# Kernel optimization log

Measured on AMD Instinct MI355X. Metric: run time of the kernel, lower is better.

The kernel has to match this reference:

```python
import jax, jax.numpy as jnp
import numpy as np

B, I, H, AH, AI = 4096, 1024, 1024, 128, 16
EPS = 1e-5  # nn.LayerNorm default


def _ln(x, w, b):
    mu = jnp.mean(x, -1, keepdims=True)
    var = jnp.mean((x - mu) ** 2, -1, keepdims=True)
    return (x - mu) * jax.lax.rsqrt(var + EPS) * w + b


def setup_inputs() -> dict:
    key = jax.random.key(0)
    ks = jax.random.split(key, 12)
    d = {}
    d['x'] = jax.random.normal(ks[0], (B, I), jnp.float32)
    d['total_h'] = jax.random.normal(ks[1], (B, H + AH), jnp.float32)
    d['total_c'] = jax.random.normal(ks[2], (B, H + AH), jnp.float32)
    # main cell params
    d['w_ih'] = jax.random.normal(ks[3], (4 * H, I), jnp.float32) * 0.02
    d['w_hh'] = jax.random.normal(ks[4], (4 * H, H), jnp.float32) * 0.02
    d['b_ih'] = jnp.zeros((4 * H,), jnp.float32)
    d['b_hh'] = jnp.zeros((4 * H,), jnp.float32)
    d['ln_i_w'] = jnp.ones((4 * H,), jnp.float32); d['ln_i_b'] = jnp.zeros((4 * H,), jnp.float32)
    d['ln_h_w'] = jnp.ones((4 * H,), jnp.float32); d['ln_h_b'] = jnp.zeros((4 * H,), jnp.float32)
    d['ln_c_w'] = jnp.ones((H,), jnp.float32); d['ln_c_b'] = jnp.zeros((H,), jnp.float32)
    # 8 AdaptiveNorm modules, stacked on leading axis (order ix,jx,fx,ox,ih,jh,fh,oh)
    d['norm_zw_w'] = jax.random.normal(ks[5], (8, AI, AH), jnp.float32) * 0.05
    d['norm_zw_b'] = jnp.ones((8, AI), jnp.float32)
    d['norm_alpha_w'] = jax.random.normal(ks[6], (8, H, AI), jnp.float32) * (0.1 / AI)
    # 8 AdaptiveBias modules, stacked (order ixb,jxb,fxb,oxb,ihb,jhb,fhb,ohb)
    d['bias_zb_w'] = jax.random.normal(ks[7], (8, AI, AH), jnp.float32) * 0.01
    d['bias_beta_w'] = jax.random.normal(ks[8], (8, H, AI), jnp.float32) * 0.01
    # adaptive LayerNormLSTMCell (input = I+H, hidden = AH)
    d['a_w_ih'] = jax.random.normal(ks[9], (4 * AH, I + H), jnp.float32) * 0.02
    d['a_w_hh'] = jax.random.normal(ks[10], (4 * AH, AH), jnp.float32) * 0.02
    d['a_ln_i_w'] = jnp.ones((4 * AH,), jnp.float32); d['a_ln_i_b'] = jnp.zeros((4 * AH,), jnp.float32)
    d['a_ln_h_w'] = jnp.ones((4 * AH,), jnp.float32); d['a_ln_h_b'] = jnp.zeros((4 * AH,), jnp.float32)
    d['a_ln_c_w'] = jnp.ones((AH,), jnp.float32); d['a_ln_c_b'] = jnp.zeros((AH,), jnp.float32)
    return d


def _forward(x, total_h, total_c, w_ih, w_hh, b_ih, b_hh, ln_i_w, ln_i_b,
             ln_h_w, ln_h_b, ln_c_w, ln_c_b, norm_zw_w, norm_zw_b,
             norm_alpha_w, bias_zb_w, bias_beta_w, a_w_ih, a_w_hh,
             a_ln_i_w, a_ln_i_b, a_ln_h_w, a_ln_h_b, a_ln_c_w, a_ln_c_b):
    hx, ah = total_h[:, :H], total_h[:, H:]
    cx, ac = total_c[:, :H], total_c[:, H:]
    # ---- adaptive LayerNormLSTMCell (hypernetwork) ----
    ai = jnp.concatenate([x, hx], axis=1)                     # [B, I+H]
    ig = _ln(ai @ a_w_ih.T, a_ln_i_w, a_ln_i_b)               # [B, 4*AH]
    hg = _ln(ah @ a_w_hh.T, a_ln_h_w, a_ln_h_b)
    g = ig + hg
    gi, gf, gj, go = jnp.split(g, 4, axis=1)                  # ingate, forget, cell, out
    acy = _ln(jax.nn.sigmoid(gf) * ac + jax.nn.sigmoid(gi) * jnp.tanh(gj), a_ln_c_w, a_ln_c_b)
    ada = jax.nn.sigmoid(go) * jnp.tanh(acy)                  # adaptive_output [B, AH]
    # ---- 8 AdaptiveNorm scales + 8 AdaptiveBias offsets, batched ----
    zw = jnp.einsum('ba,sia->bsi', ada, norm_zw_w) + norm_zw_b  # [B,8,AI]
    alpha = jnp.einsum('bsi,shi->bsh', zw, norm_alpha_w)        # [B,8,H]
    zb = jnp.einsum('ba,sia->bsi', ada, bias_zb_w)              # [B,8,AI]
    beta = jnp.einsum('bsi,shi->bsh', zb, bias_beta_w)          # [B,8,H]
    xh = (x @ w_ih.T).reshape(-1, 4, H)                         # chunks ix,jx,fx,ox
    hh = (hx @ w_hh.T).reshape(-1, 4, H)                        # chunks ih,jh,fh,oh
    in_g = (xh * alpha[:, :4] + b_ih.reshape(4, H) + beta[:, :4]).reshape(-1, 4 * H)
    hid_g = (hh * alpha[:, 4:] + b_hh.reshape(4, H) + beta[:, 4:]).reshape(-1, 4 * H)
    # ---- cell_operate ----
    gates = _ln(in_g, ln_i_w, ln_i_b) + _ln(hid_g, ln_h_w, ln_h_b)
    i, j, f, o = jnp.split(gates, 4, axis=1)                  # in, cell, forget, out
    cy = _ln(jax.nn.sigmoid(f) * cx + jax.nn.sigmoid(i) * jnp.tanh(j), ln_c_w, ln_c_b)
    hy = jax.nn.sigmoid(o) * jnp.tanh(cy)
    new_total_h = jnp.concatenate([hy, ada], axis=1)
    new_total_c = jnp.concatenate([cy, acy], axis=1)
    return hy, new_total_h, new_total_c


def reference(x, total_h, total_c, w_ih, w_hh, b_ih, b_hh, ln_i_w, ln_i_b,
              ln_h_w, ln_h_b, ln_c_w, ln_c_b, norm_zw_w, norm_zw_b,
              norm_alpha_w, bias_zb_w, bias_beta_w, a_w_ih, a_w_hh,
              a_ln_i_w, a_ln_i_b, a_ln_h_w, a_ln_h_b, a_ln_c_w, a_ln_c_b):
    return _forward(x, total_h, total_c, w_ih, w_hh, b_ih, b_hh, ln_i_w, ln_i_b,
                    ln_h_w, ln_h_b, ln_c_w, ln_c_b, norm_zw_w, norm_zw_b,
                    norm_alpha_w, bias_zb_w, bias_beta_w, a_w_ih, a_w_hh,
                    a_ln_i_w, a_ln_i_b, a_ln_h_w, a_ln_h_b, a_ln_c_w, a_ln_c_b)
```

## Files before the change

kernel.cpp:

```cpp
#include <hip/hip_runtime.h>
#include <cstdint>
#include <cstddef>


#define B_   4096
#define I_   1024
#define H_   1024
#define AH_  128
#define AI_  16
#define G4_  4096
#define EPS_ 1e-5f

#define OUT_TH ((size_t)B_ * H_)
#define OUT_TC (OUT_TH + (size_t)B_ * (H_ + AH_))

typedef short s16x8 __attribute__((ext_vector_type(8)));
typedef float f32x4 __attribute__((ext_vector_type(4)));

__device__ __forceinline__ unsigned short f2bf_rn(float f) {
    unsigned int u = __builtin_bit_cast(unsigned int, f);
    unsigned int r = u + 0x7FFFu + ((u >> 16) & 1u);
    return (unsigned short)(r >> 16);
}
__device__ __forceinline__ float bf2f(unsigned short h) {
    unsigned int u = ((unsigned int)h) << 16;
    return __builtin_bit_cast(float, u);
}
__device__ __forceinline__ float sigf(float x) { return 1.0f / (1.0f + expf(-x)); }

__device__ __forceinline__ void gld16(const void* g, void* l) {
    __builtin_amdgcn_global_load_lds(
        (const __attribute__((address_space(1))) unsigned int*)g,
        (__attribute__((address_space(3))) unsigned int*)l,
        16, 0, 0);
}

__global__ void split3_kernel(const float* __restrict__ src, int srcStride, int srcOff,
                              long total, int K,
                              unsigned short* __restrict__ dst, int dstStride,
                              int offHiA, int offHiB, int offLo) {
    long idx = (long)blockIdx.x * blockDim.x + threadIdx.x;
    if (idx >= total) return;
    int r = (int)(idx / K);
    int k = (int)(idx - (long)r * K);
    float v = src[(size_t)r * srcStride + srcOff + k];
    unsigned short hu = f2bf_rn(v);
    unsigned short lu = f2bf_rn(v - bf2f(hu));
    size_t base = (size_t)r * dstStride;
    dst[base + offHiA + k] = hu;
    dst[base + offHiB + k] = hu;
    dst[base + offLo  + k] = lu;
}

__launch_bounds__(256, 2)
__global__ void gemm_bt_bf16(const unsigned short* __restrict__ A0,
                             const unsigned short* __restrict__ A1,
                             int kSplit, int lda,
                             const unsigned short* __restrict__ W, int ldw,
                             float* __restrict__ C, int ldc, int K) {
    __shared__ __align__(16) unsigned short As[128 * 32];
    __shared__ __align__(16) unsigned short Bs[128 * 32];
    const int tid  = threadIdx.x;
    const int lane = tid & 63;
    const int w    = tid >> 6;
    const int wr   = w >> 1, wc = w & 1;
    const int bx   = blockIdx.x, by = blockIdx.y;
    const int l15  = lane & 15;
    const int lk   = (lane >> 4) * 8;

    f32x4 acc[4][4] = {};

    for (int kt = 0; kt < K; kt += 32) {
        const unsigned short* Ab = (kt < kSplit) ? (A0 + kt) : (A1 + (kt - kSplit));
        const unsigned short* Wb = W + kt;
#pragma unroll
        for (int it = 0; it < 2; ++it) {
            int q = it * 256 + tid;
            int row = q >> 2, c8 = (q & 3) * 8;
            gld16(Ab + (size_t)(by * 128 + row) * lda + c8,
                  (char*)As + (size_t)(it * 256 + w * 64) * 16);
        }
#pragma unroll
        for (int it = 0; it < 2; ++it) {
            int q = it * 256 + tid;
            int row = q >> 2, c8 = (q & 3) * 8;
            gld16(Wb + (size_t)(bx * 128 + row) * ldw + c8,
                  (char*)Bs + (size_t)(it * 256 + w * 64) * 16);
        }
        __syncthreads();

        s16x8 afr[4], bfr[4];
#pragma unroll
        for (int m = 0; m < 4; ++m)
            afr[m] = *(const s16x8*)&As[(wr * 64 + m * 16 + l15) * 32 + lk];
#pragma unroll
        for (int n = 0; n < 4; ++n)
            bfr[n] = *(const s16x8*)&Bs[(wc * 64 + n * 16 + l15) * 32 + lk];
#pragma unroll
        for (int m = 0; m < 4; ++m)
#pragma unroll
            for (int n = 0; n < 4; ++n)
                acc[m][n] = __builtin_amdgcn_mfma_f32_16x16x32_bf16(
                    afr[m], bfr[n], acc[m][n], 0, 0, 0);
        __syncthreads();
    }

    const int r0 = by * 128 + wr * 64;
    const int c0 = bx * 128 + wc * 64;
    const int rl = (lane >> 4) * 4;
#pragma unroll
    for (int m = 0; m < 4; ++m)
#pragma unroll
        for (int n = 0; n < 4; ++n)
#pragma unroll
            for (int j = 0; j < 4; ++j)
                C[(size_t)(r0 + m * 16 + rl + j) * ldc + c0 + n * 16 + l15] = acc[m][n][j];
}

__launch_bounds__(64)
__global__ void adaptive_gates_kernel(const float* __restrict__ IG, const float* __restrict__ HG,
                                      const float* __restrict__ total_c,
                                      const float* __restrict__ alniw, const float* __restrict__ alnib,
                                      const float* __restrict__ alnhw, const float* __restrict__ alnhb,
                                      const float* __restrict__ alncw, const float* __restrict__ alncb,
                                      const float* __restrict__ zw_w, const float* __restrict__ zw_b,
                                      const float* __restrict__ zb_w,
                                      float* __restrict__ ZW, float* __restrict__ ZB,
                                      float* __restrict__ out) {
    const int b    = blockIdx.x;
    const int lane = threadIdx.x;
    __shared__ float ada_lds[AH_];

    float ig[8], hg[8];
    const float* igp = IG + (size_t)b * 512 + lane * 8;
    const float* hgp = HG + (size_t)b * 512 + lane * 8;
    float sI = 0, qI = 0, sH = 0, qH = 0;
#pragma unroll
    for (int j = 0; j < 8; ++j) {
        ig[j] = igp[j]; sI += ig[j]; qI += ig[j] * ig[j];
        hg[j] = hgp[j]; sH += hg[j]; qH += hg[j] * hg[j];
    }
#pragma unroll
    for (int m = 1; m < 64; m <<= 1) {
        sI += __shfl_xor(sI, m); qI += __shfl_xor(qI, m);
        sH += __shfl_xor(sH, m); qH += __shfl_xor(qH, m);
    }
    const float muI = sI * (1.0f / 512.0f);
    const float rI  = rsqrtf(qI * (1.0f / 512.0f) - muI * muI + EPS_);
    const float muH = sH * (1.0f / 512.0f);
    const float rH  = rsqrtf(qH * (1.0f / 512.0f) - muH * muH + EPS_);

    float g[8];
#pragma unroll
    for (int j = 0; j < 8; ++j) {
        int c = lane * 8 + j;
        g[j] = (ig[j] - muI) * rI * alniw[c] + alnib[c]
             + (hg[j] - muH) * rH * alnhw[c] + alnhb[c];
    }

    const int l15 = lane & 15;
    float cp[8], gov[8];
    float s = 0, q = 0;
#pragma unroll
    for (int j = 0; j < 8; ++j) {
        float giv = __shfl(g[j], l15);
        float gfv = __shfl(g[j], 16 + l15);
        float gjv = __shfl(g[j], 32 + l15);
        gov[j]    = __shfl(g[j], 48 + l15);
        int a = l15 * 8 + j;
        float ac = total_c[(size_t)b * (H_ + AH_) + H_ + a];
        cp[j] = sigf(gfv) * ac + sigf(giv) * tanhf(gjv);
        s += cp[j]; q += cp[j] * cp[j];
    }
#pragma unroll
    for (int m = 1; m < 16; m <<= 1) { s += __shfl_xor(s, m); q += __shfl_xor(q, m); }
    const float mu = s * (1.0f / 128.0f);
    const float rs = rsqrtf(q * (1.0f / 128.0f) - mu * mu + EPS_);

    float adav[8], acyv[8];
#pragma unroll
    for (int j = 0; j < 8; ++j) {
        int a = l15 * 8 + j;
        acyv[j] = (cp[j] - mu) * rs * alncw[a] + alncb[a];
        adav[j] = sigf(gov[j]) * tanhf(acyv[j]);
    }
    if (lane < 16) {
#pragma unroll
        for (int j = 0; j < 8; ++j) {
            int a = lane * 8 + j;
            ada_lds[a] = adav[j];
            out[OUT_TH + (size_t)b * (H_ + AH_) + H_ + a] = adav[j];
            out[OUT_TC + (size_t)b * (H_ + AH_) + H_ + a] = acyv[j];
        }
    }
    __syncthreads();

#pragma unroll
    for (int t = 0; t < 2; ++t) {
        int idx = lane * 2 + t;
        const float* wz = zw_w + (size_t)idx * AH_;
        const float* wb = zb_w + (size_t)idx * AH_;
        float az = 0, ab = 0;
        for (int a = 0; a < AH_; ++a) {
            float ad = ada_lds[a];
            az += ad * wz[a];
            ab += ad * wb[a];
        }
        ZW[(size_t)b * 128 + idx] = az + zw_b[idx];
        ZB[(size_t)b * 128 + idx] = ab;
    }
}

__launch_bounds__(512)
__global__ void scale_stats_kernel(float* __restrict__ XH, float* __restrict__ HH,
                                   const float* __restrict__ ZW, const float* __restrict__ ZB,
                                   const float* __restrict__ aw, const float* __restrict__ bw,
                                   const float* __restrict__ b_ih, const float* __restrict__ b_hh,
                                   float* __restrict__ STATS) {
    const int tid  = threadIdx.x;
    const int lane = tid & 63;
    const int w    = tid >> 6;
    const int b0   = blockIdx.x * 8;

    __shared__ float zwl[8 * 128], zbl[8 * 128];
    __shared__ float part[8][8][4];
    __shared__ float tot[8][4];

    for (int t = tid; t < 1024; t += 512) {
        int r = t >> 7, si = t & 127;
        zwl[t] = ZW[(size_t)(b0 + r) * 128 + si];
        zbl[t] = ZB[(size_t)(b0 + r) * 128 + si];
    }
    __syncthreads();

    float sI[8] = {}, qI[8] = {}, sH[8] = {}, qH[8] = {};

    for (int strip = w; strip < 128; strip += 8) {
        const bool isIn = strip < 64;
        const int  c    = (isIn ? strip : strip - 64) * 64 + lane;
        const int  se   = (c >> 10) + (isIn ? 0 : 4);
        float*       X    = isIn ? XH : HH;
        const float* bias = isIn ? b_ih : b_hh;
        const int    h    = c & 1023;

        const f32x4* awp = (const f32x4*)(aw + ((size_t)se * 1024 + h) * 16);
        const f32x4* bwp = (const f32x4*)(bw + ((size_t)se * 1024 + h) * 16);
        f32x4 a0 = awp[0], a1 = awp[1], a2 = awp[2], a3 = awp[3];
        f32x4 w0 = bwp[0], w1 = bwp[1], w2 = bwp[2], w3 = bwp[3];
        const float bc = bias[c];

#pragma unroll
        for (int r = 0; r < 8; ++r) {
            const float* z  = &zwl[r * 128 + se * 16];
            const float* zb = &zbl[r * 128 + se * 16];
            float alpha = a0[0]*z[0]  + a0[1]*z[1]  + a0[2]*z[2]  + a0[3]*z[3]
                        + a1[0]*z[4]  + a1[1]*z[5]  + a1[2]*z[6]  + a1[3]*z[7]
                        + a2[0]*z[8]  + a2[1]*z[9]  + a2[2]*z[10] + a2[3]*z[11]
                        + a3[0]*z[12] + a3[1]*z[13] + a3[2]*z[14] + a3[3]*z[15];
            float beta  = w0[0]*zb[0]  + w0[1]*zb[1]  + w0[2]*zb[2]  + w0[3]*zb[3]
                        + w1[0]*zb[4]  + w1[1]*zb[5]  + w1[2]*zb[6]  + w1[3]*zb[7]
                        + w2[0]*zb[8]  + w2[1]*zb[9]  + w2[2]*zb[10] + w2[3]*zb[11]
                        + w3[0]*zb[12] + w3[1]*zb[13] + w3[2]*zb[14] + w3[3]*zb[15];
            size_t off = (size_t)(b0 + r) * G4_ + c;
            float v = X[off] * alpha + bc + beta;
            X[off] = v;
            if (isIn) { sI[r] += v; qI[r] += v * v; }
            else      { sH[r] += v; qH[r] += v * v; }
        }
    }

#pragma unroll
    for (int r = 0; r < 8; ++r) {
#pragma unroll
        for (int m = 1; m < 64; m <<= 1) {
            sI[r] += __shfl_xor(sI[r], m); qI[r] += __shfl_xor(qI[r], m);
            sH[r] += __shfl_xor(sH[r], m); qH[r] += __shfl_xor(qH[r], m);
        }
        if (lane == 0) {
            part[w][r][0] = sI[r]; part[w][r][1] = qI[r];
            part[w][r][2] = sH[r]; part[w][r][3] = qH[r];
        }
    }
    __syncthreads();
    if (tid < 32) {
        int r = tid >> 2, cmp = tid & 3;
        float t = 0;
        for (int ww = 0; ww < 8; ++ww) t += part[ww][r][cmp];
        tot[r][cmp] = t;
    }
    __syncthreads();
    if (tid < 8) {
        int r = tid;
        float muI = tot[r][0] * (1.0f / 4096.0f);
        float vI  = tot[r][1] * (1.0f / 4096.0f) - muI * muI;
        float muH = tot[r][2] * (1.0f / 4096.0f);
        float vH  = tot[r][3] * (1.0f / 4096.0f) - muH * muH;
        f32x4 st = { muI, rsqrtf(vI + EPS_), muH, rsqrtf(vH + EPS_) };
        *(f32x4*)(STATS + (size_t)(b0 + r) * 4) = st;
    }
}

__launch_bounds__(256)
__global__ void final_gates_kernel(const float* __restrict__ XH, const float* __restrict__ HH,
                                   const float* __restrict__ STATS,
                                   const float* __restrict__ lniw, const float* __restrict__ lnib,
                                   const float* __restrict__ lnhw, const float* __restrict__ lnhb,
                                   const float* __restrict__ lncw, const float* __restrict__ lncb,
                                   const float* __restrict__ total_c,
                                   float* __restrict__ out) {
    const int b = blockIdx.x, tid = threadIdx.x;
    const int lane = tid & 63, w = tid >> 6;
    __shared__ float red[4][2];

    const f32x4 st = *(const f32x4*)(STATS + (size_t)b * 4);
    const int h0 = tid * 4;

    float gg[4][4];
#pragma unroll
    for (int s = 0; s < 4; ++s) {
        int c = s * 1024 + h0;
        f32x4 xi = *(const f32x4*)(XH + (size_t)b * G4_ + c);
        f32x4 hi = *(const f32x4*)(HH + (size_t)b * G4_ + c);
        f32x4 wi = *(const f32x4*)(lniw + c);
        f32x4 bi = *(const f32x4*)(lnib + c);
        f32x4 wh = *(const f32x4*)(lnhw + c);
        f32x4 bh = *(const f32x4*)(lnhb + c);
#pragma unroll
        for (int e = 0; e < 4; ++e)
            gg[s][e] = (xi[e] - st[0]) * st[1] * wi[e] + bi[e]
                     + (hi[e] - st[2]) * st[3] * wh[e] + bh[e];
    }

    float cp[4], ov[4];
    float s_ = 0, q_ = 0;
#pragma unroll
    for (int e = 0; e < 4; ++e) {
        float iv = gg[0][e], jv = gg[1][e], fv = gg[2][e];
        ov[e] = gg[3][e];
        float cx = total_c[(size_t)b * (H_ + AH_) + h0 + e];
        cp[e] = sigf(fv) * cx + sigf(iv) * tanhf(jv);
        s_ += cp[e]; q_ += cp[e] * cp[e];
    }
#pragma unroll
    for (int m = 1; m < 64; m <<= 1) { s_ += __shfl_xor(s_, m); q_ += __shfl_xor(q_, m); }
    if (lane == 0) { red[w][0] = s_; red[w][1] = q_; }
    __syncthreads();
    float S = red[0][0] + red[1][0] + red[2][0] + red[3][0];
    float Q = red[0][1] + red[1][1] + red[2][1] + red[3][1];
    float mu = S * (1.0f / 1024.0f);
    float rs = rsqrtf(Q * (1.0f / 1024.0f) - mu * mu + EPS_);

    f32x4 hyv, cyv;
#pragma unroll
    for (int e = 0; e < 4; ++e) {
        int h = h0 + e;
        float cy = (cp[e] - mu) * rs * lncw[h] + lncb[h];
        float hy = sigf(ov[e]) * tanhf(cy);
        cyv[e] = cy; hyv[e] = hy;
    }
    *(f32x4*)(out + (size_t)b * H_ + h0)                        = hyv;
    *(f32x4*)(out + OUT_TH + (size_t)b * (H_ + AH_) + h0)       = hyv;
    *(f32x4*)(out + OUT_TC + (size_t)b * (H_ + AH_) + h0)       = cyv;
}

extern "C" void kernel_launch(void* const* d_in, const int* in_sizes, int n_in,
                              void* d_out, int out_size, void* d_ws, size_t ws_size,
                              hipStream_t stream) {
    const float* x          = (const float*)d_in[0];
    const float* total_h    = (const float*)d_in[1];
    const float* total_c    = (const float*)d_in[2];
    const float* w_ih       = (const float*)d_in[3];
    const float* w_hh       = (const float*)d_in[4];
    const float* b_ih       = (const float*)d_in[5];
    const float* b_hh       = (const float*)d_in[6];
    const float* ln_i_w     = (const float*)d_in[7];
    const float* ln_i_b     = (const float*)d_in[8];
    const float* ln_h_w     = (const float*)d_in[9];
    const float* ln_h_b     = (const float*)d_in[10];
    const float* ln_c_w     = (const float*)d_in[11];
    const float* ln_c_b     = (const float*)d_in[12];
    const float* norm_zw_w  = (const float*)d_in[13];
    const float* norm_zw_b  = (const float*)d_in[14];
    const float* norm_alpha_w = (const float*)d_in[15];
    const float* bias_zb_w  = (const float*)d_in[16];
    const float* bias_beta_w = (const float*)d_in[17];
    const float* a_w_ih     = (const float*)d_in[18];
    const float* a_w_hh     = (const float*)d_in[19];
    const float* a_ln_i_w   = (const float*)d_in[20];
    const float* a_ln_i_b   = (const float*)d_in[21];
    const float* a_ln_h_w   = (const float*)d_in[22];
    const float* a_ln_h_b   = (const float*)d_in[23];
    const float* a_ln_c_w   = (const float*)d_in[24];
    const float* a_ln_c_b   = (const float*)d_in[25];
    float* out = (float*)d_out;

    char* ws = (char*)d_ws;
    unsigned short* XA  = (unsigned short*)(ws + 0);
    unsigned short* HXA = (unsigned short*)(ws + 25165824);
    unsigned short* WIH = (unsigned short*)(ws + 50331648);
    unsigned short* WHH = (unsigned short*)(ws + 75497472);
    unsigned short* WAI = (unsigned short*)(ws + 100663296);
    unsigned short* AHS = (unsigned short*)(ws + 106954752);
    unsigned short* WAH = (unsigned short*)(ws + 110100480);
    float* IG    = (float*)(ws + 110493696);
    float* HG    = (float*)(ws + 118882304);
    float* XHp   = (float*)(ws + 127270912);
    float* HHp   = (float*)(ws + 194379776);
    float* ZW    = (float*)(ws + 261488640);
    float* ZB    = (float*)(ws + 263585792);
    float* STATS = (float*)(ws + 265682944);

    auto grid1 = [](long n) { return dim3((unsigned)((n + 255) / 256)); };

    split3_kernel<<<grid1(4096L*1024), 256, 0, stream>>>(x,       1024, 0,    4096L*1024, 1024, XA,  3072, 0, 1024, 2048);
    split3_kernel<<<grid1(4096L*1024), 256, 0, stream>>>(total_h, 1152, 0,    4096L*1024, 1024, HXA, 3072, 0, 1024, 2048);
    split3_kernel<<<grid1(4096L*128),  256, 0, stream>>>(total_h, 1152, 1024, 4096L*128,  128,  AHS, 384,  0, 128,  256);
    split3_kernel<<<grid1(4096L*1024), 256, 0, stream>>>(w_ih,    1024, 0,    4096L*1024, 1024, WIH, 3072, 0, 2048, 1024);
    split3_kernel<<<grid1(4096L*1024), 256, 0, stream>>>(w_hh,    1024, 0,    4096L*1024, 1024, WHH, 3072, 0, 2048, 1024);
    split3_kernel<<<grid1(512L*1024),  256, 0, stream>>>(a_w_ih,  2048, 0,    512L*1024,  1024, WAI,        6144, 0, 2048, 1024);
    split3_kernel<<<grid1(512L*1024),  256, 0, stream>>>(a_w_ih,  2048, 1024, 512L*1024,  1024, WAI + 3072, 6144, 0, 2048, 1024);
    split3_kernel<<<grid1(512L*128),   256, 0, stream>>>(a_w_hh,  128,  0,    512L*128,   128,  WAH, 384,  0, 256,  128);

    const int BIG = 1 << 30;
    gemm_bt_bf16<<<dim3(512/128, 4096/128), 256, 0, stream>>>(XA, HXA, 3072, 3072, WAI, 6144, IG, 512, 6144);
    gemm_bt_bf16<<<dim3(512/128, 4096/128), 256, 0, stream>>>(AHS, AHS, BIG, 384, WAH, 384, HG, 512, 384);
    gemm_bt_bf16<<<dim3(4096/128, 4096/128), 256, 0, stream>>>(XA,  XA,  BIG, 3072, WIH, 3072, XHp, 4096, 3072);
    gemm_bt_bf16<<<dim3(4096/128, 4096/128), 256, 0, stream>>>(HXA, HXA, BIG, 3072, WHH, 3072, HHp, 4096, 3072);

    adaptive_gates_kernel<<<4096, 64, 0, stream>>>(IG, HG, total_c,
        a_ln_i_w, a_ln_i_b, a_ln_h_w, a_ln_h_b, a_ln_c_w, a_ln_c_b,
        norm_zw_w, norm_zw_b, bias_zb_w, ZW, ZB, out);

    scale_stats_kernel<<<512, 512, 0, stream>>>(XHp, HHp, ZW, ZB,
        norm_alpha_w, bias_beta_w, b_ih, b_hh, STATS);

    final_gates_kernel<<<4096, 256, 0, stream>>>(XHp, HHp, STATS,
        ln_i_w, ln_i_b, ln_h_w, ln_h_b, ln_c_w, ln_c_b, total_c, out);
}
```

Measured before the change: 823.6 us.

## Vectorize bf16 split, drop duplicated hi copy, swizzle GEMM blocks, split adaptive GEMM

Result: faster. 668.6 us (-18.8%).

```diff
diff --git a/kernel.cpp b/kernel.cpp
--- a/kernel.cpp
+++ b/kernel.cpp
@@ -7,7 +7,6 @@
 #define I_   1024
 #define H_   1024
 #define AH_  128
-#define AI_  16
 #define G4_  4096
 #define EPS_ 1e-5f
 
@@ -35,44 +34,69 @@
         16, 0, 0);
 }
 
-__global__ void split3_kernel(const float* __restrict__ src, int srcStride, int srcOff,
-                              long total, int K,
+__global__ void split8_kernel(const float* __restrict__ src, int srcStride, int srcOff,
+                              long nThreads, int kshift,
                               unsigned short* __restrict__ dst, int dstStride,
-                              int offHiA, int offHiB, int offLo) {
-    long idx = (long)blockIdx.x * blockDim.x + threadIdx.x;
-    if (idx >= total) return;
-    int r = (int)(idx / K);
-    int k = (int)(idx - (long)r * K);
-    float v = src[(size_t)r * srcStride + srcOff + k];
-    unsigned short hu = f2bf_rn(v);
-    unsigned short lu = f2bf_rn(v - bf2f(hu));
-    size_t base = (size_t)r * dstStride;
-    dst[base + offHiA + k] = hu;
-    dst[base + offHiB + k] = hu;
-    dst[base + offLo  + k] = lu;
+                              int offHi, int offLo) {
+    long t = (long)blockIdx.x * blockDim.x + threadIdx.x;
+    if (t >= nThreads) return;
+    int r  = (int)(t >> kshift);
+    int kk = ((int)t & ((1 << kshift) - 1)) * 8;
+    const float* sp = src + (size_t)r * srcStride + srcOff + kk;
+    f32x4 v0 = *(const f32x4*)sp;
+    f32x4 v1 = *(const f32x4*)(sp + 4);
+    float v[8] = {v0[0], v0[1], v0[2], v0[3], v1[0], v1[1], v1[2], v1[3]};
+    s16x8 hi, lo;
+#pragma unroll
+    for (int j = 0; j < 8; ++j) {
+        unsigned short hu = f2bf_rn(v[j]);
+        unsigned short lu = f2bf_rn(v[j] - bf2f(hu));
+        hi[j] = (short)hu; lo[j] = (short)lu;
+    }
+    size_t base = (size_t)r * dstStride + kk;
+    *(s16x8*)(dst + base + offHi) = hi;
+    *(s16x8*)(dst + base + offLo) = lo;
+}
+
+__global__ void transpose128_kernel(const float* __restrict__ zw_w, const float* __restrict__ zb_w,
+                                    float* __restrict__ ZWT, float* __restrict__ ZBT) {
+    int t = blockIdx.x * 256 + threadIdx.x;
+    int idx = t >> 7, a = t & 127;
+    ZWT[a * 128 + idx] = zw_w[idx * 128 + a];
+    ZBT[a * 128 + idx] = zb_w[idx * 128 + a];
 }
 
 __launch_bounds__(256, 2)
 __global__ void gemm_bt_bf16(const unsigned short* __restrict__ A0,
                              const unsigned short* __restrict__ A1,
-                             int kSplit, int lda,
-                             const unsigned short* __restrict__ W, int ldw,
-                             float* __restrict__ C, int ldc, int K) {
+                             int lda,
+                             const unsigned short* __restrict__ W, int ldw, int wzOff,
+                             float* __restrict__ C, int ldc, long czOff,
+                             int K, int kA1, int kW1) {
     __shared__ __align__(16) unsigned short As[128 * 32];
     __shared__ __align__(16) unsigned short Bs[128 * 32];
+    const unsigned short* A  = blockIdx.z ? A1 : A0;
+    const unsigned short* Wp = W + (size_t)blockIdx.z * wzOff;
+    float* Cp = C + (size_t)blockIdx.z * czOff;
+
+    const int gx = gridDim.x;
+    int lin = blockIdx.y * gx + blockIdx.x;
+    const int cpx = (gx * gridDim.y) >> 3;
+    lin = (lin & 7) * cpx + (lin >> 3);
+    const int bx = lin % gx, by = lin / gx;
+
     const int tid  = threadIdx.x;
     const int lane = tid & 63;
     const int w    = tid >> 6;
     const int wr   = w >> 1, wc = w & 1;
-    const int bx   = blockIdx.x, by = blockIdx.y;
     const int l15  = lane & 15;
     const int lk   = (lane >> 4) * 8;
 
     f32x4 acc[4][4] = {};
 
     for (int kt = 0; kt < K; kt += 32) {
-        const unsigned short* Ab = (kt < kSplit) ? (A0 + kt) : (A1 + (kt - kSplit));
-        const unsigned short* Wb = W + kt;
+        const unsigned short* Ab = A  + (kt < kA1 ? kt : kt - kA1);
+        const unsigned short* Wb = Wp + (kt < kW1 ? kt : kt - kW1);
 #pragma unroll
         for (int it = 0; it < 2; ++it) {
             int q = it * 256 + tid;
@@ -114,17 +138,18 @@
         for (int n = 0; n < 4; ++n)
 #pragma unroll
             for (int j = 0; j < 4; ++j)
-                C[(size_t)(r0 + m * 16 + rl + j) * ldc + c0 + n * 16 + l15] = acc[m][n][j];
+                Cp[(size_t)(r0 + m * 16 + rl + j) * ldc + c0 + n * 16 + l15] = acc[m][n][j];
 }
 
 __launch_bounds__(64)
-__global__ void adaptive_gates_kernel(const float* __restrict__ IG, const float* __restrict__ HG,
+__global__ void adaptive_gates_kernel(const float* __restrict__ IGa, const float* __restrict__ IGb,
+                                      const float* __restrict__ HG,
                                       const float* __restrict__ total_c,
                                       const float* __restrict__ alniw, const float* __restrict__ alnib,
                                       const float* __restrict__ alnhw, const float* __restrict__ alnhb,
                                       const float* __restrict__ alncw, const float* __restrict__ alncb,
-                                      const float* __restrict__ zw_w, const float* __restrict__ zw_b,
-                                      const float* __restrict__ zb_w,
+                                      const float* __restrict__ ZWT, const float* __restrict__ zw_b,
+                                      const float* __restrict__ ZBT,
                                       float* __restrict__ ZW, float* __restrict__ ZB,
                                       float* __restrict__ out) {
     const int b    = blockIdx.x;
@@ -132,13 +157,14 @@
     __shared__ float ada_lds[AH_];
 
     float ig[8], hg[8];
-    const float* igp = IG + (size_t)b * 512 + lane * 8;
-    const float* hgp = HG + (size_t)b * 512 + lane * 8;
+    const float* ipa = IGa + (size_t)b * 512 + lane * 8;
+    const float* ipb = IGb + (size_t)b * 512 + lane * 8;
+    const float* hgp = HG  + (size_t)b * 512 + lane * 8;
     float sI = 0, qI = 0, sH = 0, qH = 0;
 #pragma unroll
     for (int j = 0; j < 8; ++j) {
-        ig[j] = igp[j]; sI += ig[j]; qI += ig[j] * ig[j];
-        hg[j] = hgp[j]; sH += hg[j]; qH += hg[j] * hg[j];
+        ig[j] = ipa[j] + ipb[j]; sI += ig[j]; qI += ig[j] * ig[j];
+        hg[j] = hgp[j];          sH += hg[j]; qH += hg[j] * hg[j];
     }
 #pragma unroll
     for (int m = 1; m < 64; m <<= 1) {
@@ -195,20 +221,20 @@
     }
     __syncthreads();
 
-#pragma unroll
-    for (int t = 0; t < 2; ++t) {
-        int idx = lane * 2 + t;
-        const float* wz = zw_w + (size_t)idx * AH_;
-        const float* wb = zb_w + (size_t)idx * AH_;
-        float az = 0, ab = 0;
-        for (int a = 0; a < AH_; ++a) {
-            float ad = ada_lds[a];
-            az += ad * wz[a];
-            ab += ad * wb[a];
-        }
-        ZW[(size_t)b * 128 + idx] = az + zw_b[idx];
-        ZB[(size_t)b * 128 + idx] = ab;
-    }
+    float az0 = 0, az1 = 0, ab0 = 0, ab1 = 0;
+#pragma unroll 4
+    for (int a = 0; a < 128; ++a) {
+        float ad = ada_lds[a];
+        float2 wz = *(const float2*)&ZWT[a * 128 + lane * 2];
+        float2 wb = *(const float2*)&ZBT[a * 128 + lane * 2];
+        az0 += ad * wz.x; az1 += ad * wz.y;
+        ab0 += ad * wb.x; ab1 += ad * wb.y;
+    }
+    const int i0 = lane * 2, i1 = lane * 2 + 1;
+    ZW[(size_t)b * 128 + i0] = az0 + zw_b[i0];
+    ZW[(size_t)b * 128 + i1] = az1 + zw_b[i1];
+    ZB[(size_t)b * 128 + i0] = ab0;
+    ZB[(size_t)b * 128 + i1] = ab1;
 }
 
 __launch_bounds__(512)
@@ -222,7 +248,7 @@
     const int w    = tid >> 6;
     const int b0   = blockIdx.x * 8;
 
-    __shared__ float zwl[8 * 128], zbl[8 * 128];
+    __shared__ __align__(16) float zwl[8 * 128], zbl[8 * 128];
     __shared__ float part[8][8][4];
     __shared__ float tot[8][4];
 
@@ -251,16 +277,18 @@
 
 #pragma unroll
         for (int r = 0; r < 8; ++r) {
-            const float* z  = &zwl[r * 128 + se * 16];
-            const float* zb = &zbl[r * 128 + se * 16];
-            float alpha = a0[0]*z[0]  + a0[1]*z[1]  + a0[2]*z[2]  + a0[3]*z[3]
-                        + a1[0]*z[4]  + a1[1]*z[5]  + a1[2]*z[6]  + a1[3]*z[7]
-                        + a2[0]*z[8]  + a2[1]*z[9]  + a2[2]*z[10] + a2[3]*z[11]
-                        + a3[0]*z[12] + a3[1]*z[13] + a3[2]*z[14] + a3[3]*z[15];
-            float beta  = w0[0]*zb[0]  + w0[1]*zb[1]  + w0[2]*zb[2]  + w0[3]*zb[3]
-                        + w1[0]*zb[4]  + w1[1]*zb[5]  + w1[2]*zb[6]  + w1[3]*zb[7]
-                        + w2[0]*zb[8]  + w2[1]*zb[9]  + w2[2]*zb[10] + w2[3]*zb[11]
-                        + w3[0]*zb[12] + w3[1]*zb[13] + w3[2]*zb[14] + w3[3]*zb[15];
+            const f32x4* zp = (const f32x4*)&zwl[r * 128 + se * 16];
+            const f32x4* yp = (const f32x4*)&zbl[r * 128 + se * 16];
+            f32x4 z0 = zp[0], z1 = zp[1], z2 = zp[2], z3 = zp[3];
+            f32x4 y0 = yp[0], y1 = yp[1], y2 = yp[2], y3 = yp[3];
+            float alpha = a0[0]*z0[0] + a0[1]*z0[1] + a0[2]*z0[2] + a0[3]*z0[3]
+                        + a1[0]*z1[0] + a1[1]*z1[1] + a1[2]*z1[2] + a1[3]*z1[3]
+                        + a2[0]*z2[0] + a2[1]*z2[1] + a2[2]*z2[2] + a2[3]*z2[3]
+                        + a3[0]*z3[0] + a3[1]*z3[1] + a3[2]*z3[2] + a3[3]*z3[3];
+            float beta  = w0[0]*y0[0] + w0[1]*y0[1] + w0[2]*y0[2] + w0[3]*y0[3]
+                        + w1[0]*y1[0] + w1[1]*y1[1] + w1[2]*y1[2] + w1[3]*y1[3]
+                        + w2[0]*y2[0] + w2[1]*y2[1] + w2[2]*y2[2] + w2[3]*y2[3]
+                        + w3[0]*y3[0] + w3[1]*y3[1] + w3[2]*y3[2] + w3[3]*y3[3];
             size_t off = (size_t)(b0 + r) * G4_ + c;
             float v = X[off] * alpha + bc + beta;
             X[off] = v;
@@ -358,9 +386,9 @@
         float hy = sigf(ov[e]) * tanhf(cy);
         cyv[e] = cy; hyv[e] = hy;
     }
-    *(f32x4*)(out + (size_t)b * H_ + h0)                        = hyv;
-    *(f32x4*)(out + OUT_TH + (size_t)b * (H_ + AH_) + h0)       = hyv;
-    *(f32x4*)(out + OUT_TC + (size_t)b * (H_ + AH_) + h0)       = cyv;
+    *(f32x4*)(out + (size_t)b * H_ + h0)                  = hyv;
+    *(f32x4*)(out + OUT_TH + (size_t)b * (H_ + AH_) + h0) = hyv;
+    *(f32x4*)(out + OUT_TC + (size_t)b * (H_ + AH_) + h0) = cyv;
 }
 
 extern "C" void kernel_launch(void* const* d_in, const int* in_sizes, int n_in,
@@ -396,40 +424,42 @@
 
     char* ws = (char*)d_ws;
     unsigned short* XA  = (unsigned short*)(ws + 0);
-    unsigned short* HXA = (unsigned short*)(ws + 25165824);
-    unsigned short* WIH = (unsigned short*)(ws + 50331648);
-    unsigned short* WHH = (unsigned short*)(ws + 75497472);
-    unsigned short* WAI = (unsigned short*)(ws + 100663296);
-    unsigned short* AHS = (unsigned short*)(ws + 106954752);
-    unsigned short* WAH = (unsigned short*)(ws + 110100480);
-    float* IG    = (float*)(ws + 110493696);
-    float* HG    = (float*)(ws + 118882304);
-    float* XHp   = (float*)(ws + 127270912);
-    float* HHp   = (float*)(ws + 194379776);
-    float* ZW    = (float*)(ws + 261488640);
-    float* ZB    = (float*)(ws + 263585792);
-    float* STATS = (float*)(ws + 265682944);
-
-    auto grid1 = [](long n) { return dim3((unsigned)((n + 255) / 256)); };
-
-    split3_kernel<<<grid1(4096L*1024), 256, 0, stream>>>(x,       1024, 0,    4096L*1024, 1024, XA,  3072, 0, 1024, 2048);
-    split3_kernel<<<grid1(4096L*1024), 256, 0, stream>>>(total_h, 1152, 0,    4096L*1024, 1024, HXA, 3072, 0, 1024, 2048);
-    split3_kernel<<<grid1(4096L*128),  256, 0, stream>>>(total_h, 1152, 1024, 4096L*128,  128,  AHS, 384,  0, 128,  256);
-    split3_kernel<<<grid1(4096L*1024), 256, 0, stream>>>(w_ih,    1024, 0,    4096L*1024, 1024, WIH, 3072, 0, 2048, 1024);
-    split3_kernel<<<grid1(4096L*1024), 256, 0, stream>>>(w_hh,    1024, 0,    4096L*1024, 1024, WHH, 3072, 0, 2048, 1024);
-    split3_kernel<<<grid1(512L*1024),  256, 0, stream>>>(a_w_ih,  2048, 0,    512L*1024,  1024, WAI,        6144, 0, 2048, 1024);
-    split3_kernel<<<grid1(512L*1024),  256, 0, stream>>>(a_w_ih,  2048, 1024, 512L*1024,  1024, WAI + 3072, 6144, 0, 2048, 1024);
-    split3_kernel<<<grid1(512L*128),   256, 0, stream>>>(a_w_hh,  128,  0,    512L*128,   128,  WAH, 384,  0, 256,  128);
-
-    const int BIG = 1 << 30;
-    gemm_bt_bf16<<<dim3(512/128, 4096/128), 256, 0, stream>>>(XA, HXA, 3072, 3072, WAI, 6144, IG, 512, 6144);
-    gemm_bt_bf16<<<dim3(512/128, 4096/128), 256, 0, stream>>>(AHS, AHS, BIG, 384, WAH, 384, HG, 512, 384);
-    gemm_bt_bf16<<<dim3(4096/128, 4096/128), 256, 0, stream>>>(XA,  XA,  BIG, 3072, WIH, 3072, XHp, 4096, 3072);
-    gemm_bt_bf16<<<dim3(4096/128, 4096/128), 256, 0, stream>>>(HXA, HXA, BIG, 3072, WHH, 3072, HHp, 4096, 3072);
-
-    adaptive_gates_kernel<<<4096, 64, 0, stream>>>(IG, HG, total_c,
+    unsigned short* HXA = (unsigned short*)(ws + 16777216);
+    unsigned short* WIH = (unsigned short*)(ws + 33554432);
+    unsigned short* WHH = (unsigned short*)(ws + 50331648);
+    unsigned short* WAI = (unsigned short*)(ws + 67108864);
+    unsigned short* AHS = (unsigned short*)(ws + 71303168);
+    unsigned short* WAH = (unsigned short*)(ws + 73400320);
+    float* IG    = (float*)(ws + 73662464);
+    float* HG    = (float*)(ws + 90439680);
+    float* XHp   = (float*)(ws + 98828288);
+    float* HHp   = (float*)(ws + 165937152);
+    float* ZW    = (float*)(ws + 233046016);
+    float* ZB    = (float*)(ws + 235143168);
+    float* STATS = (float*)(ws + 237240320);
+    float* ZWT   = (float*)(ws + 237305856);
+    float* ZBT   = (float*)(ws + 237371392);
+
+    auto grid8 = [](long n) { return dim3((unsigned)((n / 8 + 255) / 256)); };
+
+    split8_kernel<<<grid8(4096L*1024), 256, 0, stream>>>(x,       1024, 0,    4096L*128, 7, XA,  2048, 0, 1024);
+    split8_kernel<<<grid8(4096L*1024), 256, 0, stream>>>(total_h, 1152, 0,    4096L*128, 7, HXA, 2048, 0, 1024);
+    split8_kernel<<<grid8(4096L*128),  256, 0, stream>>>(total_h, 1152, 1024, 4096L*16,  4, AHS, 256,  0, 128);
+    split8_kernel<<<grid8(4096L*1024), 256, 0, stream>>>(w_ih,    1024, 0,    4096L*128, 7, WIH, 2048, 0, 1024);
+    split8_kernel<<<grid8(4096L*1024), 256, 0, stream>>>(w_hh,    1024, 0,    4096L*128, 7, WHH, 2048, 0, 1024);
+    split8_kernel<<<grid8(512L*1024),  256, 0, stream>>>(a_w_ih,  2048, 0,    512L*128,  7, WAI, 4096, 0,    1024);
+    split8_kernel<<<grid8(512L*1024),  256, 0, stream>>>(a_w_ih,  2048, 1024, 512L*128,  7, WAI, 4096, 2048, 3072);
+    split8_kernel<<<grid8(512L*128),   256, 0, stream>>>(a_w_hh,  128,  0,    512L*16,   4, WAH, 256,  0, 128);
+    transpose128_kernel<<<64, 256, 0, stream>>>(norm_zw_w, bias_zb_w, ZWT, ZBT);
+
+    gemm_bt_bf16<<<dim3(4, 32, 2), 256, 0, stream>>>(XA, HXA, 2048, WAI, 4096, 2048, IG, 512, 4096L*512, 3072, 1024, 2048);
+    gemm_bt_bf16<<<dim3(4, 32, 1), 256, 0, stream>>>(AHS, AHS, 256, WAH, 256, 0, HG, 512, 0, 384, 128, 256);
+    gemm_bt_bf16<<<dim3(32, 32, 1), 256, 0, stream>>>(XA,  XA,  2048, WIH, 2048, 0, XHp, 4096, 0, 3072, 1024, 2048);
+    gemm_bt_bf16<<<dim3(32, 32, 1), 256, 0, stream>>>(HXA, HXA, 2048, WHH, 2048, 0, HHp, 4096, 0, 3072, 1024, 2048);
+
+    adaptive_gates_kernel<<<4096, 64, 0, stream>>>(IG, IG + 4096L*512, HG, total_c,
         a_ln_i_w, a_ln_i_b, a_ln_h_w, a_ln_h_b, a_ln_c_w, a_ln_c_b,
-        norm_zw_w, norm_zw_b, bias_zb_w, ZW, ZB, out);
+        ZWT, norm_zw_b, ZBT, ZW, ZB, out);
 
     scale_stats_kernel<<<512, 512, 0, stream>>>(XHp, HHp, ZW, ZB,
         norm_alpha_w, bias_beta_w, b_ih, b_hh, STATS);
```
